# Performance work log

Hardware: AMD Instinct MI355X
Metric: run time of the kernel (lower is better)

## Reference

```python
import jax, jax.numpy as jnp
import numpy as np

N = 100000   # nodes
E = 1600000  # edges
IN = 128
HID = 128
OUT = 40
EPS = 1e-5


def setup_inputs() -> dict:
    key = jax.random.key(0)
    ks = jax.random.split(key, 8)
    x = jax.random.normal(ks[0], (N, IN), jnp.float32)
    edge_index = jax.random.randint(ks[1], (2, E), 0, N, dtype=jnp.int32)
    W1 = jax.random.normal(ks[2], (IN, HID), jnp.float32) / np.float32(np.sqrt(IN))
    b1 = jnp.zeros((HID,), jnp.float32)
    g1 = jnp.ones((HID,), jnp.float32)
    be1 = jnp.zeros((HID,), jnp.float32)
    W2 = jax.random.normal(ks[3], (HID, HID), jnp.float32) / np.float32(np.sqrt(HID))
    b2 = jnp.zeros((HID,), jnp.float32)
    g2 = jnp.ones((HID,), jnp.float32)
    be2 = jnp.zeros((HID,), jnp.float32)
    W3 = jax.random.normal(ks[4], (HID, OUT), jnp.float32) / np.float32(np.sqrt(HID))
    b3 = jnp.zeros((OUT,), jnp.float32)
    return dict(x=x, edge_index=edge_index, W1=W1, b1=b1, g1=g1, be1=be1,
                W2=W2, b2=b2, g2=g2, be2=be2, W3=W3, b3=b3)


def _gcn_norm(edge_index, n):
    # PyG gcn_norm: add self loops, symmetric D^-1/2 (A+I) D^-1/2 weights
    loop = jnp.arange(n, dtype=edge_index.dtype)
    src = jnp.concatenate([edge_index[0], loop])
    dst = jnp.concatenate([edge_index[1], loop])
    deg = jax.ops.segment_sum(jnp.ones_like(dst, jnp.float32), dst, num_segments=n)
    dinv = jnp.where(deg > 0, jax.lax.rsqrt(deg), 0.0)
    norm = dinv[src] * dinv[dst]  # [E+N]
    return src, dst, norm


def _gcn_conv(x, W, b, src, dst, norm, n):
    h = x @ W                                   # [N, F]
    msg = h[src] * norm[:, None]                # gather + scale  [E+N, F]
    agg = jax.ops.segment_sum(msg, dst, num_segments=n)
    return agg + b


def _batchnorm(x, g, be):
    mu = jnp.mean(x, axis=0)
    var = jnp.var(x, axis=0)
    return (x - mu) * jax.lax.rsqrt(var + EPS) * g + be


def reference(x, edge_index, W1, b1, g1, be1, W2, b2, g2, be2, W3, b3):
    n = x.shape[0]
    src, dst, norm = _gcn_norm(edge_index, n)
    h = _gcn_conv(x, W1, b1, src, dst, norm, n)
    h = jax.nn.relu(_batchnorm(h, g1, be1))
    h = _gcn_conv(h, W2, b2, src, dst, norm, n)
    h = jax.nn.relu(_batchnorm(h, g2, be2))
    h = _gcn_conv(h, W3, b3, src, dst, norm, n)
    return jax.nn.softmax(h, axis=-1)
```

## Files before the change

kernel.cpp:

```cpp
#include <hip/hip_runtime.h>
#include <hip/hip_fp16.h>

#define NN   100000
#define NE   1600000
#define NBUCK 391
#define NW1   512
#define CH1   (NE / NW1)
#define GN    (NBUCK * NW1)
#define SC    512
#define SNB   (GN / SC)
#define BNB   512
constexpr float EPSV = 1e-5f;

typedef _Float16 f16x8 __attribute__((ext_vector_type(8)));
typedef float    f32x4 __attribute__((ext_vector_type(4)));


__global__ __launch_bounds__(256) void p1hist_kernel(const int* __restrict__ dst,
                                                     int* __restrict__ G) {
    __shared__ int h[NBUCK];
    int t = threadIdx.x, wg = blockIdx.x;
    for (int i = t; i < NBUCK; i += 256) h[i] = 0;
    __syncthreads();
    int base = wg * CH1;
    for (int e = base + t; e < base + CH1; e += 256)
        atomicAdd(&h[dst[e] >> 8], 1);
    __syncthreads();
    for (int i = t; i < NBUCK; i += 256) G[i * NW1 + wg] = h[i];
}

__global__ __launch_bounds__(256) void gscan1_kernel(const int* __restrict__ G,
                                                     int* __restrict__ bsum) {
    __shared__ int red[256];
    int t = threadIdx.x;
    int base = blockIdx.x * SC + t * 2;
    red[t] = G[base] + G[base + 1];
    __syncthreads();
    #pragma unroll
    for (int off = 128; off > 0; off >>= 1) {
        if (t < off) red[t] += red[t + off];
        __syncthreads();
    }
    if (t == 0) bsum[blockIdx.x] = red[0];
}

__global__ __launch_bounds__(512) void gscan2_kernel(const int* __restrict__ bsum,
                                                     int* __restrict__ boff) {
    __shared__ int s[512];
    int t = threadIdx.x;
    int v = (t < SNB) ? bsum[t] : 0;
    s[t] = v;
    __syncthreads();
    #pragma unroll
    for (int off = 1; off < 512; off <<= 1) {
        int u = (t >= off) ? s[t - off] : 0;
        __syncthreads();
        s[t] += u;
        __syncthreads();
    }
    if (t < SNB) boff[t] = s[t] - v;
}

__global__ __launch_bounds__(256) void gscan3_kernel(int* __restrict__ G,
                                                     const int* __restrict__ boff) {
    __shared__ int s[256];
    int t = threadIdx.x;
    int base = blockIdx.x * SC + t * 2;
    int c0 = G[base], c1 = G[base + 1];
    int pair = c0 + c1;
    s[t] = pair;
    __syncthreads();
    #pragma unroll
    for (int off = 1; off < 256; off <<= 1) {
        int u = (t >= off) ? s[t - off] : 0;
        __syncthreads();
        s[t] += u;
        __syncthreads();
    }
    int excl = boff[blockIdx.x] + s[t] - pair;
    G[base]     = excl;
    G[base + 1] = excl + c0;
}

__global__ __launch_bounds__(256) void p1fill_kernel(const int* __restrict__ src,
                                                     const int* __restrict__ dst,
                                                     const int* __restrict__ G,
                                                     int* __restrict__ ebuf) {
    __shared__ int cur[NBUCK];
    int t = threadIdx.x, wg = blockIdx.x;
    for (int i = t; i < NBUCK; i += 256) cur[i] = G[i * NW1 + wg];
    __syncthreads();
    int base = wg * CH1;
    for (int e = base + t; e < base + CH1; e += 256) {
        int d = dst[e];
        int pos = atomicAdd(&cur[d >> 8], 1);
        ebuf[pos] = src[e] | ((d & 255) << 17);
    }
}

__global__ __launch_bounds__(256) void p2build_kernel(const int* __restrict__ ebuf,
                                                      const int* __restrict__ G,
                                                      int* __restrict__ rowptr,
                                                      int* __restrict__ srcsorted,
                                                      float* __restrict__ dinv) {
    __shared__ int cnt[256];
    __shared__ int s[256];
    __shared__ int cur[256];
    int t = threadIdx.x, b = blockIdx.x;
    int base = G[b * NW1];
    int endp = (b == NBUCK - 1) ? NE : G[(b + 1) * NW1];
    cnt[t] = 0;
    __syncthreads();
    for (int e = base + t; e < endp; e += 256)
        atomicAdd(&cnt[ebuf[e] >> 17], 1);
    __syncthreads();
    int c = cnt[t];
    s[t] = c;
    __syncthreads();
    #pragma unroll
    for (int off = 1; off < 256; off <<= 1) {
        int u = (t >= off) ? s[t - off] : 0;
        __syncthreads();
        s[t] += u;
        __syncthreads();
    }
    int excl = s[t] - c;
    int node = b * 256 + t;
    if (node < NN) {
        rowptr[node] = base + excl;
        dinv[node]   = rsqrtf((float)c + 1.0f);
    }
    cur[t] = base + excl;
    __syncthreads();
    for (int e = base + t; e < endp; e += 256) {
        int p = ebuf[e];
        int pos = atomicAdd(&cur[p >> 17], 1);
        srcsorted[pos] = p & 0x1FFFF;
    }
    if (b == NBUCK - 1 && t == 0) rowptr[NN] = NE;
}


__global__ void wprep_kernel(const float* __restrict__ W1, const float* __restrict__ W2,
                             __half* __restrict__ Wt) {
    int b = blockIdx.x;
    int layer = b >> 7, n = b & 127, k = threadIdx.x;
    const float* W = layer ? W2 : W1;
    Wt[layer * 16384 + n * 128 + k] = __float2half_rn(W[k * 128 + n]);
}


__global__ __launch_bounds__(256) void bnstats_kernel(const __half* __restrict__ X,
                                                      float* __restrict__ partial) {
    __shared__ float red[4][256];
    int t = threadIdx.x;
    int f2 = t & 63, rg = t >> 6;
    const __half2* base = (const __half2*)X + f2;
    float s0 = 0.f, s1 = 0.f, q0 = 0.f, q1 = 0.f;
    for (int r = blockIdx.x * 4 + rg; r < NN; r += BNB * 4) {
        float2 v = __half22float2(base[(size_t)r * 64]);
        s0 += v.x; s1 += v.y; q0 += v.x * v.x; q1 += v.y * v.y;
    }
    red[rg][f2 * 4 + 0] = s0;
    red[rg][f2 * 4 + 1] = s1;
    red[rg][f2 * 4 + 2] = q0;
    red[rg][f2 * 4 + 3] = q1;
    __syncthreads();
    int kind = t >> 7, f = t & 127;
    int slot = (f >> 1) * 4 + (f & 1) + kind * 2;
    float v = red[0][slot] + red[1][slot] + red[2][slot] + red[3][slot];
    partial[blockIdx.x * 256 + kind * 128 + f] = v;
}

__global__ __launch_bounds__(256) void bnfinal_kernel(const float* __restrict__ partial,
                                                      const float* __restrict__ g,
                                                      const float* __restrict__ be,
                                                      float* __restrict__ sc) {
    __shared__ float red[256];
    int t = threadIdx.x;
    float v = 0.f;
    #pragma unroll 8
    for (int sl = 0; sl < BNB; ++sl) v += partial[sl * 256 + t];
    red[t] = v;
    __syncthreads();
    if (t < 128) {
        float s = red[t], q = red[128 + t];
        float mu  = s * (1.0f / NN);
        float var = q * (1.0f / NN) - mu * mu;
        float rstd = rsqrtf(var + EPSV);
        float scale = g[t] * rstd;
        sc[t]       = scale;
        sc[128 + t] = be[t] - mu * scale;
    }
}


__device__ __forceinline__ int swzb(int row, int colByte) {
    return row * 256 + (colByte ^ ((row & 7) << 4));
}

template<bool BN, typename TIN>
__global__ __launch_bounds__(256) void gemm128m_kernel(const TIN* __restrict__ X,
        const __half* __restrict__ Wt, const float* __restrict__ sc,
        const float* __restrict__ dinv, __half* __restrict__ Y) {
    __shared__ __align__(16) char Xs[64 * 256];
    __shared__ __align__(16) char Wts[128 * 256];
    __shared__ float dvs[64];
    int tid = threadIdx.x;
    int node0 = blockIdx.x * 64;

    {
        int n = tid >> 1, c0 = (tid & 1) * 64;
        const _Float16* g = (const _Float16*)Wt + n * 128 + c0;
        #pragma unroll
        for (int j = 0; j < 8; ++j) {
            f16x8 v = *(const f16x8*)(g + j * 8);
            *(f16x8*)(Wts + swzb(n, (c0 + j * 8) * 2)) = v;
        }
    }
    {
        int r = tid >> 2, c0 = (tid & 3) * 32;
        int grow = node0 + r;
        #pragma unroll
        for (int j = 0; j < 4; ++j) {
            int c = c0 + j * 8;
            f16x8 o;
            if (grow < NN) {
                float f[8];
                if constexpr (sizeof(TIN) == 4) {
                    float4 u0 = *(const float4*)((const float*)X + (size_t)grow * 128 + c);
                    float4 u1 = *(const float4*)((const float*)X + (size_t)grow * 128 + c + 4);
                    f[0] = u0.x; f[1] = u0.y; f[2] = u0.z; f[3] = u0.w;
                    f[4] = u1.x; f[5] = u1.y; f[6] = u1.z; f[7] = u1.w;
                } else {
                    f16x8 h = *(const f16x8*)((const _Float16*)X + (size_t)grow * 128 + c);
                    #pragma unroll
                    for (int i = 0; i < 8; ++i) f[i] = (float)h[i];
                }
                #pragma unroll
                for (int i = 0; i < 8; ++i) {
                    if constexpr (BN) f[i] = fmaxf(fmaf(f[i], sc[c + i], sc[128 + c + i]), 0.f);
                    o[i] = (_Float16)f[i];
                }
            } else {
                #pragma unroll
                for (int i = 0; i < 8; ++i) o[i] = (_Float16)0.f;
            }
            *(f16x8*)(Xs + swzb(r, c * 2)) = o;
        }
    }
    if (tid < 64) dvs[tid] = (node0 + tid < NN) ? dinv[node0 + tid] : 0.f;
    __syncthreads();

    int lane = tid & 63;
    int wv   = tid >> 6;
    int n0w  = wv * 32;
    int lm   = lane & 15;
    int lg   = lane >> 4;

    f32x4 acc[4][2] = {};
    #pragma unroll
    for (int s = 0; s < 4; ++s) {
        int kb = (s * 32 + lg * 8) * 2;
        f16x8 a[4], b[2];
        #pragma unroll
        for (int i = 0; i < 4; ++i)
            a[i] = *(const f16x8*)(Xs + swzb(i * 16 + lm, kb));
        #pragma unroll
        for (int r = 0; r < 2; ++r)
            b[r] = *(const f16x8*)(Wts + swzb(n0w + r * 16 + lm, kb));
        #pragma unroll
        for (int i = 0; i < 4; ++i)
            #pragma unroll
            for (int r = 0; r < 2; ++r)
                acc[i][r] = __builtin_amdgcn_mfma_f32_16x16x32_f16(a[i], b[r], acc[i][r], 0, 0, 0);
    }

    _Float16* Yh = (_Float16*)Y;
    #pragma unroll
    for (int i = 0; i < 4; ++i) {
        #pragma unroll
        for (int q = 0; q < 4; ++q) {
            int row = i * 16 + lg * 4 + q;
            int grow = node0 + row;
            if (grow < NN) {
                float di = dvs[row];
                Yh[(size_t)grow * 128 + n0w + lm]      = (_Float16)(acc[i][0][q] * di);
                Yh[(size_t)grow * 128 + n0w + 16 + lm] = (_Float16)(acc[i][1][q] * di);
            }
        }
    }
}


__global__ __launch_bounds__(256) void gemm40_kernel(const __half* __restrict__ X,
        const float* __restrict__ W, const float* __restrict__ sc,
        const float* __restrict__ dinv, __half* __restrict__ Y) {
    __shared__ float Ws[128][40];
    __shared__ float Xs[32][132];
    int tx = threadIdx.x, ty = threadIdx.y;
    int tid = ty * 8 + tx;
    int node0 = blockIdx.x * 32;

    float* wf = &Ws[0][0];
    for (int idx = tid; idx < 128 * 40; idx += 256) wf[idx] = W[idx];
    for (int idx = tid * 8; idx < 32 * 128; idx += 256 * 8) {
        int n = idx >> 7, f = idx & 127;
        f16x8 h = *(const f16x8*)((const _Float16*)X + (size_t)(node0 + n) * 128 + f);
        float v[8];
        #pragma unroll
        for (int i = 0; i < 8; ++i)
            v[i] = fmaxf(fmaf((float)h[i], sc[f + i], sc[128 + f + i]), 0.f);
        *(float4*)&Xs[n][f]     = make_float4(v[0], v[1], v[2], v[3]);
        *(float4*)&Xs[n][f + 4] = make_float4(v[4], v[5], v[6], v[7]);
    }
    __syncthreads();

    float acc[5] = {0, 0, 0, 0, 0};
    int f0 = tx * 5;
    #pragma unroll 4
    for (int k = 0; k < 128; ++k) {
        float xv = Xs[ty][k];
        #pragma unroll
        for (int j = 0; j < 5; ++j) acc[j] = fmaf(xv, Ws[k][f0 + j], acc[j]);
    }
    float di = dinv[node0 + ty];
    __half* yp = Y + (size_t)(node0 + ty) * 64;
    #pragma unroll
    for (int j = 0; j < 5; ++j) yp[f0 + j] = __float2half_rn(acc[j] * di);
    #pragma unroll
    for (int j = 0; j < 3; ++j) yp[40 + tx * 3 + j] = __float2half_rn(0.f);
}


__global__ __launch_bounds__(256) void agg128_kernel(const __half* __restrict__ H,
        const int* __restrict__ rowptr, const int* __restrict__ srcs,
        const float* __restrict__ dinv, const float* __restrict__ bias,
        __half* __restrict__ Bout) {
    int wave = threadIdx.x >> 6;
    int lane = threadIdx.x & 63;
    int node = blockIdx.x * 4 + wave;
    int beg = rowptr[node], end = rowptr[node + 1];
    int g = lane >> 4;
    int c = lane & 15;
    const f16x8* Hc = (const f16x8*)H + c;
    float acc[8] = {};
    int e = beg;
    for (; e + 7 < end; e += 8) {
        int s0 = srcs[e + g];
        int s1 = srcs[e + 4 + g];
        f16x8 h0 = Hc[(size_t)s0 * 16];
        f16x8 h1 = Hc[(size_t)s1 * 16];
        #pragma unroll
        for (int j = 0; j < 8; ++j) acc[j] += (float)h0[j] + (float)h1[j];
    }
    for (; e + 3 < end; e += 4) {
        int s0 = srcs[e + g];
        f16x8 h0 = Hc[(size_t)s0 * 16];
        #pragma unroll
        for (int j = 0; j < 8; ++j) acc[j] += (float)h0[j];
    }
    if (e + g < end) {
        int s = srcs[e + g];
        f16x8 h = Hc[(size_t)s * 16];
        #pragma unroll
        for (int j = 0; j < 8; ++j) acc[j] += (float)h[j];
    }
    #pragma unroll
    for (int j = 0; j < 8; ++j) {
        acc[j] += __shfl_xor(acc[j], 16);
        acc[j] += __shfl_xor(acc[j], 32);
    }
    float di = dinv[node];
    f16x8 hs = Hc[(size_t)node * 16];
    _Float16 o[8];
    #pragma unroll
    for (int j = 0; j < 8; ++j) {
        float v = di * (acc[j] + (float)hs[j]) + bias[c * 8 + j];
        o[j] = (_Float16)v;
    }
    if (g == 0)
        *((f16x8*)Bout + (size_t)node * 16 + c) = *(f16x8*)o;
}


__global__ __launch_bounds__(256) void agg40_softmax_kernel(const __half* __restrict__ H,
        const int* __restrict__ rowptr, const int* __restrict__ srcs,
        const float* __restrict__ dinv, const float* __restrict__ bias,
        float* __restrict__ out) {
    int wave = threadIdx.x >> 6;
    int lane = threadIdx.x & 63;
    int node = blockIdx.x * 4 + wave;
    int beg = rowptr[node], end = rowptr[node + 1];
    bool act = lane < 40;
    const _Float16* Hc = (const _Float16*)H + lane;
    float a0 = 0.f, a1 = 0.f, a2 = 0.f, a3 = 0.f;
    float a4 = 0.f, a5 = 0.f, a6 = 0.f, a7 = 0.f;
    int e = beg;
    for (; e + 7 < end; e += 8) {
        a0 += (float)Hc[(size_t)srcs[e]     * 64];
        a1 += (float)Hc[(size_t)srcs[e + 1] * 64];
        a2 += (float)Hc[(size_t)srcs[e + 2] * 64];
        a3 += (float)Hc[(size_t)srcs[e + 3] * 64];
        a4 += (float)Hc[(size_t)srcs[e + 4] * 64];
        a5 += (float)Hc[(size_t)srcs[e + 5] * 64];
        a6 += (float)Hc[(size_t)srcs[e + 6] * 64];
        a7 += (float)Hc[(size_t)srcs[e + 7] * 64];
    }
    if (e + 3 < end) {
        a0 += (float)Hc[(size_t)srcs[e]     * 64];
        a1 += (float)Hc[(size_t)srcs[e + 1] * 64];
        a2 += (float)Hc[(size_t)srcs[e + 2] * 64];
        a3 += (float)Hc[(size_t)srcs[e + 3] * 64];
        e += 4;
    }
    for (; e < end; ++e) a0 += (float)Hc[(size_t)srcs[e] * 64];
    float di = dinv[node];
    float hs = (float)Hc[(size_t)node * 64];
    float v = act ? (di * (a0 + a1 + a2 + a3 + a4 + a5 + a6 + a7 + hs) + bias[lane]) : -3.0e38f;
    float m = v;
    #pragma unroll
    for (int off = 32; off > 0; off >>= 1) m = fmaxf(m, __shfl_xor(m, off));
    float ev = act ? expf(v - m) : 0.f;
    float ssum = ev;
    #pragma unroll
    for (int off = 32; off > 0; off >>= 1) ssum += __shfl_xor(ssum, off);
    if (act) out[(size_t)node * 40 + lane] = ev / ssum;
}


extern "C" void kernel_launch(void* const* d_in, const int* in_sizes, int n_in,
                              void* d_out, int out_size, void* d_ws, size_t ws_size,
                              hipStream_t stream) {
    const float* x   = (const float*)d_in[0];
    const int*   ei  = (const int*)d_in[1];
    const float* W1  = (const float*)d_in[2];
    const float* b1  = (const float*)d_in[3];
    const float* g1  = (const float*)d_in[4];
    const float* be1 = (const float*)d_in[5];
    const float* W2  = (const float*)d_in[6];
    const float* b2  = (const float*)d_in[7];
    const float* g2  = (const float*)d_in[8];
    const float* be2 = (const float*)d_in[9];
    const float* W3  = (const float*)d_in[10];
    const float* b3  = (const float*)d_in[11];
    float* out = (float*)d_out;
    const int* src = ei;
    const int* dst = ei + NE;

    char* p = (char*)d_ws;
    auto alloc = [&](size_t bytes) { char* r = p; p += (bytes + 255) & ~255ull; return r; };
    int*    rowptr    = (int*)   alloc((size_t)(NN + 1) * 4);
    int*    srcsorted = (int*)   alloc((size_t)NE * 4);
    float*  dinv      = (float*) alloc((size_t)NN * 4);
    float*  sc        = (float*) alloc(256 * 4);
    int*    G         = (int*)   alloc((size_t)GN * 4);
    int*    bsum      = (int*)   alloc((size_t)SNB * 4);
    int*    boff      = (int*)   alloc((size_t)SNB * 4);
    float*  partial   = (float*) alloc((size_t)BNB * 256 * 4);
    __half* Wth       = (__half*)alloc((size_t)2 * 16384 * 2);
    __half* A         = (__half*)alloc((size_t)NN * 128 * 2);
    __half* Bh        = (__half*)alloc((size_t)NN * 128 * 2);
    int*    ebuf      = (int*)A;

    wprep_kernel<<<256, 128, 0, stream>>>(W1, W2, Wth);
    p1hist_kernel<<<NW1, 256, 0, stream>>>(dst, G);
    gscan1_kernel<<<SNB, 256, 0, stream>>>(G, bsum);
    gscan2_kernel<<<1, 512, 0, stream>>>(bsum, boff);
    gscan3_kernel<<<SNB, 256, 0, stream>>>(G, boff);
    p1fill_kernel<<<NW1, 256, 0, stream>>>(src, dst, G, ebuf);
    p2build_kernel<<<NBUCK, 256, 0, stream>>>(ebuf, G, rowptr, srcsorted, dinv);

    const int GB = (NN + 63) / 64;
    gemm128m_kernel<false, float><<<GB, 256, 0, stream>>>(x, Wth, nullptr, dinv, A);
    agg128_kernel<<<NN / 4, 256, 0, stream>>>(A, rowptr, srcsorted, dinv, b1, Bh);
    bnstats_kernel<<<BNB, 256, 0, stream>>>(Bh, partial);
    bnfinal_kernel<<<1, 256, 0, stream>>>(partial, g1, be1, sc);
    gemm128m_kernel<true, __half><<<GB, 256, 0, stream>>>(Bh, Wth + 16384, sc, dinv, A);
    agg128_kernel<<<NN / 4, 256, 0, stream>>>(A, rowptr, srcsorted, dinv, b2, Bh);
    bnstats_kernel<<<BNB, 256, 0, stream>>>(Bh, partial);
    bnfinal_kernel<<<1, 256, 0, stream>>>(partial, g2, be2, sc);
    gemm40_kernel<<<NN / 32, dim3(8, 32), 0, stream>>>(Bh, W3, sc, dinv, A);
    agg40_softmax_kernel<<<NN / 4, 256, 0, stream>>>(A, rowptr, srcsorted, dinv, b3, out);
}
```

Measured before the change: 402.8 us.

## Fold block-offset scan into gscan3, pack layer-3 features to 40 halves, use fma accumulation

The separate single-block gscan2 launch is removed. Each gscan3 block now recomputes its own offset by reducing the preceding bsum entries, which saves a launch at the cost of redundant small reductions. The layer-3 feature buffer is stored with a row stride of 40 halves instead of 64, with no zero padding, so the final aggregation gathers fewer bytes per row, though rows are no longer 128-byte aligned. Accumulations are rewritten as fmaf with 1.0, and inactive lanes are clamped to column 0.

```diff
diff --git a/kernel.cpp b/kernel.cpp
--- a/kernel.cpp
+++ b/kernel.cpp
@@ -44,27 +44,21 @@
     if (t == 0) bsum[blockIdx.x] = red[0];
 }
 
-__global__ __launch_bounds__(512) void gscan2_kernel(const int* __restrict__ bsum,
-                                                     int* __restrict__ boff) {
-    __shared__ int s[512];
-    int t = threadIdx.x;
-    int v = (t < SNB) ? bsum[t] : 0;
-    s[t] = v;
-    __syncthreads();
-    #pragma unroll
-    for (int off = 1; off < 512; off <<= 1) {
-        int u = (t >= off) ? s[t - off] : 0;
-        __syncthreads();
-        s[t] += u;
-        __syncthreads();
-    }
-    if (t < SNB) boff[t] = s[t] - v;
-}
-
 __global__ __launch_bounds__(256) void gscan3_kernel(int* __restrict__ G,
-                                                     const int* __restrict__ boff) {
+                                                     const int* __restrict__ bsum) {
+    __shared__ int pre[256];
     __shared__ int s[256];
     int t = threadIdx.x;
+    int part = 0;
+    for (int j = t; j < (int)blockIdx.x; j += 256) part += bsum[j];
+    pre[t] = part;
+    __syncthreads();
+    #pragma unroll
+    for (int off = 128; off > 0; off >>= 1) {
+        if (t < off) pre[t] += pre[t + off];
+        __syncthreads();
+    }
+    int boffv = pre[0];
     int base = blockIdx.x * SC + t * 2;
     int c0 = G[base], c1 = G[base + 1];
     int pair = c0 + c1;
@@ -77,7 +71,7 @@
         s[t] += u;
         __syncthreads();
     }
-    int excl = boff[blockIdx.x] + s[t] - pair;
+    int excl = boffv + s[t] - pair;
     G[base]     = excl;
     G[base + 1] = excl + c0;
 }
@@ -325,11 +319,9 @@
         for (int j = 0; j < 5; ++j) acc[j] = fmaf(xv, Ws[k][f0 + j], acc[j]);
     }
     float di = dinv[node0 + ty];
-    __half* yp = Y + (size_t)(node0 + ty) * 64;
+    __half* yp = Y + (size_t)(node0 + ty) * 40;
     #pragma unroll
     for (int j = 0; j < 5; ++j) yp[f0 + j] = __float2half_rn(acc[j] * di);
-    #pragma unroll
-    for (int j = 0; j < 3; ++j) yp[40 + tx * 3 + j] = __float2half_rn(0.f);
 }
 
 
@@ -352,19 +344,22 @@
         f16x8 h0 = Hc[(size_t)s0 * 16];
         f16x8 h1 = Hc[(size_t)s1 * 16];
         #pragma unroll
-        for (int j = 0; j < 8; ++j) acc[j] += (float)h0[j] + (float)h1[j];
+        for (int j = 0; j < 8; ++j) {
+            acc[j] = fmaf((float)h0[j], 1.0f, acc[j]);
+            acc[j] = fmaf((float)h1[j], 1.0f, acc[j]);
+        }
     }
     for (; e + 3 < end; e += 4) {
         int s0 = srcs[e + g];
         f16x8 h0 = Hc[(size_t)s0 * 16];
         #pragma unroll
-        for (int j = 0; j < 8; ++j) acc[j] += (float)h0[j];
+        for (int j = 0; j < 8; ++j) acc[j] = fmaf((float)h0[j], 1.0f, acc[j]);
     }
     if (e + g < end) {
         int s = srcs[e + g];
         f16x8 h = Hc[(size_t)s * 16];
         #pragma unroll
-        for (int j = 0; j < 8; ++j) acc[j] += (float)h[j];
+        for (int j = 0; j < 8; ++j) acc[j] = fmaf((float)h[j], 1.0f, acc[j]);
     }
     #pragma unroll
     for (int j = 0; j < 8; ++j) {
@@ -393,30 +388,31 @@
     int node = blockIdx.x * 4 + wave;
     int beg = rowptr[node], end = rowptr[node + 1];
     bool act = lane < 40;
-    const _Float16* Hc = (const _Float16*)H + lane;
+    int ln = act ? lane : 0;
+    const _Float16* Hc = (const _Float16*)H + ln;
     float a0 = 0.f, a1 = 0.f, a2 = 0.f, a3 = 0.f;
     float a4 = 0.f, a5 = 0.f, a6 = 0.f, a7 = 0.f;
     int e = beg;
     for (; e + 7 < end; e += 8) {
-        a0 += (float)Hc[(size_t)srcs[e]     * 64];
-        a1 += (float)Hc[(size_t)srcs[e + 1] * 64];
-        a2 += (float)Hc[(size_t)srcs[e + 2] * 64];
-        a3 += (float)Hc[(size_t)srcs[e + 3] * 64];
-        a4 += (float)Hc[(size_t)srcs[e + 4] * 64];
-        a5 += (float)Hc[(size_t)srcs[e + 5] * 64];
-        a6 += (float)Hc[(size_t)srcs[e + 6] * 64];
-        a7 += (float)Hc[(size_t)srcs[e + 7] * 64];
+        a0 = fmaf((float)Hc[(size_t)srcs[e]     * 40], 1.0f, a0);
+        a1 = fmaf((float)Hc[(size_t)srcs[e + 1] * 40], 1.0f, a1);
+        a2 = fmaf((float)Hc[(size_t)srcs[e + 2] * 40], 1.0f, a2);
+        a3 = fmaf((float)Hc[(size_t)srcs[e + 3] * 40], 1.0f, a3);
+        a4 = fmaf((float)Hc[(size_t)srcs[e + 4] * 40], 1.0f, a4);
+        a5 = fmaf((float)Hc[(size_t)srcs[e + 5] * 40], 1.0f, a5);
+        a6 = fmaf((float)Hc[(size_t)srcs[e + 6] * 40], 1.0f, a6);
+        a7 = fmaf((float)Hc[(size_t)srcs[e + 7] * 40], 1.0f, a7);
     }
     if (e + 3 < end) {
-        a0 += (float)Hc[(size_t)srcs[e]     * 64];
-        a1 += (float)Hc[(size_t)srcs[e + 1] * 64];
-        a2 += (float)Hc[(size_t)srcs[e + 2] * 64];
-        a3 += (float)Hc[(size_t)srcs[e + 3] * 64];
+        a0 = fmaf((float)Hc[(size_t)srcs[e]     * 40], 1.0f, a0);
+        a1 = fmaf((float)Hc[(size_t)srcs[e + 1] * 40], 1.0f, a1);
+        a2 = fmaf((float)Hc[(size_t)srcs[e + 2] * 40], 1.0f, a2);
+        a3 = fmaf((float)Hc[(size_t)srcs[e + 3] * 40], 1.0f, a3);
         e += 4;
     }
-    for (; e < end; ++e) a0 += (float)Hc[(size_t)srcs[e] * 64];
+    for (; e < end; ++e) a0 = fmaf((float)Hc[(size_t)srcs[e] * 40], 1.0f, a0);
     float di = dinv[node];
-    float hs = (float)Hc[(size_t)node * 64];
+    float hs = (float)Hc[(size_t)node * 40];
     float v = act ? (di * (a0 + a1 + a2 + a3 + a4 + a5 + a6 + a7 + hs) + bias[lane]) : -3.0e38f;
     float m = v;
     #pragma unroll
@@ -456,7 +452,6 @@
     float*  sc        = (float*) alloc(256 * 4);
     int*    G         = (int*)   alloc((size_t)GN * 4);
     int*    bsum      = (int*)   alloc((size_t)SNB * 4);
-    int*    boff      = (int*)   alloc((size_t)SNB * 4);
     float*  partial   = (float*) alloc((size_t)BNB * 256 * 4);
     __half* Wth       = (__half*)alloc((size_t)2 * 16384 * 2);
     __half* A         = (__half*)alloc((size_t)NN * 128 * 2);
@@ -466,8 +461,7 @@
     wprep_kernel<<<256, 128, 0, stream>>>(W1, W2, Wth);
     p1hist_kernel<<<NW1, 256, 0, stream>>>(dst, G);
     gscan1_kernel<<<SNB, 256, 0, stream>>>(G, bsum);
-    gscan2_kernel<<<1, 512, 0, stream>>>(bsum, boff);
-    gscan3_kernel<<<SNB, 256, 0, stream>>>(G, boff);
+    gscan3_kernel<<<SNB, 256, 0, stream>>>(G, bsum);
     p1fill_kernel<<<NW1, 256, 0, stream>>>(src, dst, G, ebuf);
     p2build_kernel<<<NBUCK, 256, 0, stream>>>(ebuf, G, rowptr, srcsorted, dinv);
 
```

Result: no change. 401.3 us (-0.4%).
